# Kernel optimization log

Measured on AMD Instinct MI355X. Metric: run time of the kernel, lower is better.

## Reference

```python
import jax, jax.numpy as jnp
import numpy as np
from jax import lax

B, L, D_MODEL = 2, 1024, 2048
D_INNER, D_STATE, D_CONV, DT_RANK = 4096, 16, 4, 128
EPS = 1e-5


def setup_inputs() -> dict:
    key = jax.random.key(0)
    ks = jax.random.split(key, 10)
    sc = lambda k, shape, s=0.02: jax.random.normal(k, shape, jnp.float32) * s
    # A initialized like real Mamba: A_log = log(arange(1, d_state+1))
    A_log = jnp.log(jnp.broadcast_to(jnp.arange(1, D_STATE + 1, dtype=jnp.float32), (D_INNER, D_STATE)))
    return {
        "hidden_states": jax.random.normal(ks[0], (B, L, D_MODEL), jnp.float32),
        "residual": jax.random.normal(ks[1], (B, L, D_MODEL), jnp.float32),
        "norm_weight": jnp.ones((D_MODEL,), jnp.float32),
        "in_proj_w": sc(ks[2], (2 * D_INNER, D_MODEL)),
        "conv_w": sc(ks[3], (D_INNER, D_CONV), 0.1),
        "conv_b": jnp.zeros((D_INNER,), jnp.float32),
        "x_proj_w": sc(ks[4], (DT_RANK + 2 * D_STATE, D_INNER)),
        "dt_proj_w": sc(ks[5], (D_INNER, DT_RANK), 0.1),
        "dt_proj_b": sc(ks[6], (D_INNER,), 0.5),
        "A_log": A_log,
        "D_param": jnp.ones((D_INNER,), jnp.float32),
        "out_proj_w": sc(ks[7], (D_MODEL, D_INNER)),
    }


def _rmsnorm(x, w, eps=EPS):
    var = jnp.mean(jnp.square(x), axis=-1, keepdims=True)
    return x * lax.rsqrt(var + eps) * w


def _mamba_block(hidden_states, residual, norm_weight, in_proj_w, conv_w, conv_b,
                 x_proj_w, dt_proj_w, dt_proj_b, A_log, D_param, out_proj_w):
    # fused add + RMSNorm, residual kept in fp32 (prenorm=True)
    residual = (hidden_states + residual).astype(jnp.float32)
    hs = _rmsnorm(residual, norm_weight)

    # ---- Mamba mixer ----
    xz = jnp.einsum("bld,ed->ble", hs, in_proj_w)          # [B,L,2*d_inner]
    x, z = jnp.split(xz, 2, axis=-1)                        # each [B,L,d_inner]

    # depthwise causal conv over time
    xt = x.swapaxes(1, 2)                                   # [B,d_inner,L]
    xt = lax.conv_general_dilated(
        xt, conv_w[:, None, :], window_strides=(1,), padding=[(D_CONV - 1, 0)],
        dimension_numbers=("NCH", "OIH", "NCH"), feature_group_count=D_INNER)
    xt = xt + conv_b[:, None]
    x = jax.nn.silu(xt).swapaxes(1, 2)                      # [B,L,d_inner]

    # input-dependent dt, B, C
    x_dbl = jnp.einsum("bld,ed->ble", x, x_proj_w)          # [B,L,dt_rank+2*d_state]
    dt, Bm, Cm = jnp.split(x_dbl, [DT_RANK, DT_RANK + D_STATE], axis=-1)
    dt = jax.nn.softplus(jnp.einsum("blr,dr->bld", dt, dt_proj_w) + dt_proj_b)  # [B,L,d_inner]

    A = -jnp.exp(A_log)                                     # [d_inner,d_state]

    # selective scan: h_t = exp(dt_t*A) h_{t-1} + dt_t*B_t*x_t ; y_t = <h_t, C_t>
    def step(h, inp):
        dt_t, x_t, B_t, C_t = inp                           # [B,di],[B,di],[B,ds],[B,ds]
        dA = jnp.exp(dt_t[:, :, None] * A)                  # [B,di,ds]
        h = dA * h + (dt_t * x_t)[:, :, None] * B_t[:, None, :]
        y = jnp.einsum("bds,bs->bd", h, C_t)
        return h, y

    xs = (dt.swapaxes(0, 1), x.swapaxes(0, 1), Bm.swapaxes(0, 1), Cm.swapaxes(0, 1))
    h0 = jnp.zeros((B, D_INNER, D_STATE), jnp.float32)
    _, ys = lax.scan(step, h0, xs)                          # ys: [L,B,d_inner]
    y = ys.swapaxes(0, 1) + x * D_param                     # [B,L,d_inner]

    y = y * jax.nn.silu(z)
    out = jnp.einsum("bld,ed->ble", y, out_proj_w)          # [B,L,d_model]
    return out, residual


def reference(hidden_states, residual, norm_weight, in_proj_w, conv_w, conv_b,
              x_proj_w, dt_proj_w, dt_proj_b, A_log, D_param, out_proj_w):
    return _mamba_block(hidden_states, residual, norm_weight, in_proj_w, conv_w,
                        conv_b, x_proj_w, dt_proj_w, dt_proj_b, A_log, D_param,
                        out_proj_w)
```

## Files before the change

### kernel.cpp

```cpp
#include <hip/hip_runtime.h>
#include <hip/hip_bf16.h>
#include <math.h>

#define B_SZ    2
#define L_SZ    1024
#define DMODEL  2048
#define DINNER  4096
#define DSTATE  16
#define DCONV   4
#define DTRANK  128
#define NROWS   (B_SZ * L_SZ)
#define NCHUNK  16
#define CHUNKLEN (L_SZ / NCHUNK)

typedef __hip_bfloat16 bf16;
typedef __attribute__((ext_vector_type(8))) short  short8;
typedef __attribute__((ext_vector_type(4))) float  floatx4;

static __device__ __forceinline__ float b2f(bf16 v) { return __bfloat162float(v); }
static __device__ __forceinline__ bf16  f2b(float v) { return __float2bfloat16(v); }

static __device__ __forceinline__ void cvt8(const short8 v, float* out) {
    #pragma unroll
    for (int i = 0; i < 8; i++) {
        unsigned int u = ((unsigned int)(unsigned short)v[i]) << 16;
        out[i] = __builtin_bit_cast(float, u);
    }
}

static __device__ __forceinline__ float softplus_safe(float x) {
    return fmaxf(x, 0.f) + log1pf(__expf(-fabsf(x)));
}

static __device__ __forceinline__ void gload_lds16(const bf16* g, bf16* l) {
    __builtin_amdgcn_global_load_lds(
        (const __attribute__((address_space(1))) void*)g,
        (__attribute__((address_space(3))) void*)l,
        16, 0, 0);
}

__global__ void probe_kernel(const void* nw, int* flag) {
    if (threadIdx.x == 0 && blockIdx.x == 0) {
        const unsigned short* p = (const unsigned short*)nw;
        *flag = (p[0] == 0x3F80u) ? 0 : 1;
    }
}
__global__ void assert_fp32_kernel(const int* flag, float* out) {
    if (*flag == 0) out[blockIdx.x * 256 + threadIdx.x] = 888.0f;
}
__global__ void fill_diag_kernel(unsigned short* out, int n) {
    int i = blockIdx.x * 256 + threadIdx.x;
    if (i < n) out[i] = 0x4442;
}

__global__ __launch_bounds__(256) void cvt_w_kernel(
    const float* __restrict__ in, bf16* __restrict__ out, int n)
{
    int i = (blockIdx.x * 256 + threadIdx.x) * 4;
    if (i < n) {
        float4 v = *(const float4*)(in + i);
        out[i + 0] = f2b(v.x); out[i + 1] = f2b(v.y);
        out[i + 2] = f2b(v.z); out[i + 3] = f2b(v.w);
    }
}

__global__ __launch_bounds__(256) void addnorm_kernel(
    const float* __restrict__ h, const float* __restrict__ r,
    const float* __restrict__ w, bf16* __restrict__ hs_out)
{
    const int row = blockIdx.x;
    const int t   = threadIdx.x;
    const size_t base = (size_t)row * DMODEL;

    float vals[8];
    float ss = 0.f;
    #pragma unroll
    for (int i = 0; i < 8; i++) {
        int c = t + i * 256;
        float v = h[base + c] + r[base + c];
        vals[i] = v;
        ss += v * v;
    }
    #pragma unroll
    for (int off = 32; off > 0; off >>= 1) ss += __shfl_down(ss, off);
    __shared__ float wsum[4];
    if ((t & 63) == 0) wsum[t >> 6] = ss;
    __syncthreads();
    float tot = wsum[0] + wsum[1] + wsum[2] + wsum[3];
    float scale = rsqrtf(tot / (float)DMODEL + 1e-5f);

    #pragma unroll
    for (int i = 0; i < 8; i++) {
        int c = t + i * 256;
        hs_out[base + c] = f2b(vals[i] * scale * w[c]);
    }
}

__global__ __launch_bounds__(256) void residual_out_kernel(
    const float* __restrict__ h, const float* __restrict__ r,
    float* __restrict__ resp)
{
    int i = (blockIdx.x * 256 + threadIdx.x) * 4;
    float4 a = *(const float4*)(h + i);
    float4 b = *(const float4*)(r + i);
    float4 o = {a.x + b.x, a.y + b.y, a.z + b.z, a.w + b.w};
    *(float4*)(resp + i) = o;
}

__global__ __launch_bounds__(256) void addf_kernel(
    float* __restrict__ outp, const float* __restrict__ c1)
{
    int i = (blockIdx.x * 256 + threadIdx.x) * 4;
    float4 a = *(const float4*)(outp + i);
    float4 b = *(const float4*)(c1 + i);
    float4 o = {a.x + b.x, a.y + b.y, a.z + b.z, a.w + b.w};
    *(float4*)(outp + i) = o;
}

__global__ __launch_bounds__(512, 2) void gemm_bigtile(
    const bf16* __restrict__ A, const bf16* __restrict__ B,
    bf16* __restrict__ C, int N, int K, int lda, int ldb, int ldc)
{
    __shared__ bf16 sA[4][8192];
    __shared__ bf16 sB[4][8192];

    const int t     = threadIdx.x;
    const int lane  = t & 63;
    const int w     = t >> 6;
    const int wm    = w & 1;
    const int wn    = w >> 1;
    const int idx16 = lane & 15;
    const int quad  = lane >> 4;

    const int tilesN = N >> 8;
    const int m_blk  = (blockIdx.x / tilesN) << 8;
    const int n_blk  = (blockIdx.x % tilesN) << 8;

    const int srow  = t >> 2;
    const int sslot = t & 3;
    const int gswz  = ((sslot ^ ((srow >> 1) & 3)) << 3);
    const bf16* gA = A + (size_t)(m_blk + srow) * lda + gswz;
    const bf16* gB = B + (size_t)(n_blk + srow) * ldb + gswz;

    bf16* ldsA = &sA[0][0] + (w << 9);
    bf16* ldsB = &sB[0][0] + (w << 9);

    const int rswz = ((quad ^ ((idx16 >> 1) & 3)) << 3);
    const int aoff = ((wm << 7) + idx16) * 32 + rswz;
    const int boff = ((wn << 6) + idx16) * 32 + rswz;

#define STAGE_A(tt) do { const int _r = (tt) & 3; const size_t _k = (size_t)(tt) << 5; \
    gload_lds16(gA + _k,                      ldsA + _r * 8192); \
    gload_lds16(gA + ((size_t)lda << 7) + _k, ldsA + _r * 8192 + 4096); } while (0)
#define STAGE_B(tt) do { const int _r = (tt) & 3; const size_t _k = (size_t)(tt) << 5; \
    gload_lds16(gB + _k,                      ldsB + _r * 8192); \
    gload_lds16(gB + ((size_t)ldb << 7) + _k, ldsB + _r * 8192 + 4096); } while (0)

    floatx4 acc[8][4] = {};
    const int NT = K >> 5;

    STAGE_A(0); STAGE_B(0);
    STAGE_A(1); STAGE_B(1);
    STAGE_A(2); STAGE_B(2);
    asm volatile("s_waitcnt vmcnt(8)" ::: "memory");
    __builtin_amdgcn_s_barrier();
    __builtin_amdgcn_sched_barrier(0);

    #pragma unroll 1
    for (int tt = 0; tt < NT; ++tt) {
        const bf16* la = &sA[tt & 3][0] + aoff;
        const bf16* lb = &sB[tt & 3][0] + boff;

        short8 af[4], bfr[4];
        #pragma unroll
        for (int i = 0; i < 4; i++) af[i]  = *(const short8*)(la + i * 512);
        #pragma unroll
        for (int j = 0; j < 4; j++) bfr[j] = *(const short8*)(lb + j * 512);
        if (tt + 3 < NT) STAGE_A(tt + 3);
        asm volatile("s_waitcnt lgkmcnt(0)" ::: "memory");
        __builtin_amdgcn_sched_barrier(0);
        __builtin_amdgcn_s_setprio(1);
        #pragma unroll
        for (int i = 0; i < 4; i++)
            #pragma unroll
            for (int j = 0; j < 4; j++)
                acc[i][j] = __builtin_amdgcn_mfma_f32_16x16x32_bf16(
                    af[i], bfr[j], acc[i][j], 0, 0, 0);
        __builtin_amdgcn_s_setprio(0);

        short8 ag[4];
        #pragma unroll
        for (int i = 0; i < 4; i++) ag[i] = *(const short8*)(la + (i + 4) * 512);
        if (tt + 3 < NT) STAGE_B(tt + 3);
        asm volatile("s_waitcnt lgkmcnt(0)" ::: "memory");
        __builtin_amdgcn_sched_barrier(0);
        __builtin_amdgcn_s_setprio(1);
        #pragma unroll
        for (int i = 0; i < 4; i++)
            #pragma unroll
            for (int j = 0; j < 4; j++)
                acc[i + 4][j] = __builtin_amdgcn_mfma_f32_16x16x32_bf16(
                    ag[i], bfr[j], acc[i + 4][j], 0, 0, 0);
        __builtin_amdgcn_s_setprio(0);

        const int ahead = NT - 1 - tt;
        if (ahead >= 3)      asm volatile("s_waitcnt vmcnt(8)" ::: "memory");
        else if (ahead == 2) asm volatile("s_waitcnt vmcnt(4)" ::: "memory");
        else if (ahead == 1) asm volatile("s_waitcnt vmcnt(0)" ::: "memory");
        if (ahead > 0) {
            __builtin_amdgcn_s_barrier();
            __builtin_amdgcn_sched_barrier(0);
        }
    }
#undef STAGE_A
#undef STAGE_B

    #pragma unroll
    for (int i = 0; i < 8; i++) {
        #pragma unroll
        for (int j = 0; j < 4; j++) {
            const int r0 = m_blk + (wm << 7) + i * 16 + quad * 4;
            const int c  = n_blk + (wn << 6) + j * 16 + idx16;
            #pragma unroll
            for (int rr = 0; rr < 4; rr++)
                C[(size_t)(r0 + rr) * ldc + c] = f2b(acc[i][j][rr]);
        }
    }
}

__global__ __launch_bounds__(256) void gemm_lds_sk2(
    const bf16* __restrict__ A, const bf16* __restrict__ B,
    float* __restrict__ C0, float* __restrict__ C1)
{
    __shared__ bf16 As[128 * 32];
    __shared__ bf16 Bs[128 * 32];

    const int t    = threadIdx.x;
    const int lane = t & 63;
    const int wave = t >> 6;
    const int ks   = blockIdx.x >> 8;
    const int bid  = blockIdx.x & 255;
    const int m_blk = (bid >> 4) * 128;
    const int n_blk = (bid & 15) * 128;
    const int kbase = ks * 2048;

    const int idx16 = lane & 15;
    const int quad  = lane >> 4;
    const int wm = (wave & 1) * 64;
    const int wn = (wave >> 1) * 64;

    const int row_s = t >> 2;
    const int koff  = ((t & 3) ^ ((row_s >> 1) & 3)) * 8;
    const bf16* gA = A + (size_t)(m_blk + row_s) * 4096 + koff + kbase;
    const bf16* gB = B + (size_t)(n_blk + row_s) * 4096 + koff + kbase;
    bf16* lA = As + wave * 512;
    bf16* lB = Bs + wave * 512;

    const int rswz = (quad ^ ((idx16 >> 1) & 3)) * 8;

    floatx4 acc[4][4] = {};

    for (int k0 = 0; k0 < 2048; k0 += 32) {
        gload_lds16(gA + k0,                    lA);
        gload_lds16(gA + (size_t)64 * 4096 + k0, lA + 2048);
        gload_lds16(gB + k0,                    lB);
        gload_lds16(gB + (size_t)64 * 4096 + k0, lB + 2048);
        __syncthreads();

        short8 af[4], bfr[4];
        #pragma unroll
        for (int i = 0; i < 4; i++)
            af[i]  = *(const short8*)(As + (wm + i * 16 + idx16) * 32 + rswz);
        #pragma unroll
        for (int j = 0; j < 4; j++)
            bfr[j] = *(const short8*)(Bs + (wn + j * 16 + idx16) * 32 + rswz);
        #pragma unroll
        for (int i = 0; i < 4; i++)
            #pragma unroll
            for (int j = 0; j < 4; j++)
                acc[i][j] = __builtin_amdgcn_mfma_f32_16x16x32_bf16(
                    af[i], bfr[j], acc[i][j], 0, 0, 0);
        __syncthreads();
    }

    float* C = ks ? C1 : C0;
    #pragma unroll
    for (int i = 0; i < 4; i++) {
        #pragma unroll
        for (int j = 0; j < 4; j++) {
            const int r0 = m_blk + wm + i * 16 + quad * 4;
            const int c  = n_blk + wn + j * 16 + idx16;
            #pragma unroll
            for (int r = 0; r < 4; r++)
                C[(size_t)(r0 + r) * DMODEL + c] = acc[i][j][r];
        }
    }
}

__global__ __launch_bounds__(256) void gemm_g2_sk(
    const bf16* __restrict__ x, const bf16* __restrict__ W,
    float* __restrict__ part)
{
    const int lane = threadIdx.x & 63;
    const int gw   = blockIdx.x * 4 + (threadIdx.x >> 6);
    const int tile = gw >> 2;
    const int s    = gw & 3;
    const int wm = tile / 10;
    const int wn = tile % 10;
    const int idx16 = lane & 15, quad = lane >> 4;
    const int k0 = s * 1024;

    floatx4 acc = {};
    const bf16* Ap = x + (size_t)(wm * 16 + idx16) * DINNER + quad * 8 + k0;
    const bf16* Bp = W + (size_t)(wn * 16 + idx16) * DINNER + quad * 8 + k0;
    for (int k = 0; k < 1024; k += 32) {
        short8 af  = *(const short8*)(Ap + k);
        short8 bfr = *(const short8*)(Bp + k);
        acc = __builtin_amdgcn_mfma_f32_16x16x32_bf16(af, bfr, acc, 0, 0, 0);
    }
    #pragma unroll
    for (int r = 0; r < 4; r++)
        part[((size_t)s * NROWS + wm * 16 + quad * 4 + r) * 160 + wn * 16 + idx16]
            = acc[r];
}

__global__ __launch_bounds__(256) void g2_reduce_kernel(
    const float* __restrict__ part, bf16* __restrict__ xdbl)
{
    int i = blockIdx.x * 256 + threadIdx.x;
    float v = part[i] + part[327680 + i] + part[2 * 327680 + i]
            + part[3 * 327680 + i];
    xdbl[i] = f2b(v);
}

__global__ __launch_bounds__(256) void gemm_g3_direct(
    const bf16* __restrict__ xdbl, const bf16* __restrict__ W,
    const float* __restrict__ bias, bf16* __restrict__ dtout)
{
    const int lane = threadIdx.x & 63;
    const int gw   = blockIdx.x * 4 + (threadIdx.x >> 6);
    const int wm = gw >> 8;
    const int wn = gw & 255;
    const int idx16 = lane & 15, quad = lane >> 4;

    floatx4 acc = {};
    const bf16* Ap = xdbl + (size_t)(wm * 16 + idx16) * 160 + quad * 8;
    const bf16* Bp = W + (size_t)(wn * 16 + idx16) * DTRANK + quad * 8;
    #pragma unroll
    for (int k = 0; k < 128; k += 32) {
        short8 af  = *(const short8*)(Ap + k);
        short8 bfr = *(const short8*)(Bp + k);
        acc = __builtin_amdgcn_mfma_f32_16x16x32_bf16(af, bfr, acc, 0, 0, 0);
    }
    const int c = wn * 16 + idx16;
    const float bv = bias[c];
    #pragma unroll
    for (int r = 0; r < 4; r++)
        dtout[(size_t)(wm * 16 + quad * 4 + r) * (2 * DINNER) + c]
            = f2b(softplus_safe(acc[r] + bv));
}

__global__ __launch_bounds__(256) void conv_silu_kernel(
    const bf16* __restrict__ xz, const float* __restrict__ cw,
    const float* __restrict__ cb, bf16* __restrict__ xout)
{
    const int idx = (blockIdx.x * 256 + threadIdx.x) * 8;
    const int d0 = idx & (DINNER - 1);
    const int bl = idx >> 12;
    const int l  = bl & (L_SZ - 1);
    const int b  = bl >> 10;

    float acc[8];
    {
        float4 c0 = *(const float4*)(cb + d0);
        float4 c1 = *(const float4*)(cb + d0 + 4);
        acc[0] = c0.x; acc[1] = c0.y; acc[2] = c0.z; acc[3] = c0.w;
        acc[4] = c1.x; acc[5] = c1.y; acc[6] = c1.z; acc[7] = c1.w;
    }
    floatx4 cwv[8];
    #pragma unroll
    for (int i = 0; i < 8; i++)
        cwv[i] = *(const floatx4*)(cw + (size_t)(d0 + i) * DCONV);

    #pragma unroll
    for (int t = 0; t < DCONV; t++) {
        int ls = l - (DCONV - 1) + t;
        if (ls >= 0) {
            short8 v = *(const short8*)(xz + ((size_t)(b * L_SZ + ls)) * (2 * DINNER) + d0);
            float xf[8]; cvt8(v, xf);
            #pragma unroll
            for (int i = 0; i < 8; i++) acc[i] += cwv[i][t] * xf[i];
        }
    }
    short8 o;
    #pragma unroll
    for (int i = 0; i < 8; i++) {
        float s = acc[i] / (1.f + __expf(-acc[i]));
        o[i] = (short)__builtin_bit_cast(unsigned short, f2b(s));
    }
    *(short8*)(xout + idx) = o;
}

__global__ __launch_bounds__(256) void scan_part1(
    const bf16* __restrict__ xz, const bf16* __restrict__ x,
    const bf16* __restrict__ xdbl, const float* __restrict__ A_log,
    float* __restrict__ hpart, float* __restrict__ dtsum)
{
    __shared__ float sBC[64 * 32];
    const int tid = threadIdx.x, bid = blockIdx.x;
    const int sub = tid & 1;
    const int d   = ((bid & 31) << 7) + (tid >> 1);
    const int b   = (bid >> 5) & 1;
    const int c   = bid >> 6;
    const size_t row0 = (size_t)b * L_SZ + c * CHUNKLEN;

    {
        int r = tid >> 2, sl = tid & 3;
        short8 v = *(const short8*)(xdbl + (row0 + r) * 160 + DTRANK + sl * 8);
        float tmp[8]; cvt8(v, tmp);
        #pragma unroll
        for (int i = 0; i < 8; i++) sBC[r * 32 + sl * 8 + i] = tmp[i];
    }
    __syncthreads();

    float Aa[8];
    #pragma unroll
    for (int s = 0; s < 8; s++)
        Aa[s] = -__expf(A_log[d * DSTATE + sub * 8 + s]);

    float h[8] = {};
    float dts = 0.f;
    const floatx4* BC4 = (const floatx4*)sBC;
    const int bc0 = sub * 2;

    #pragma unroll 1
    for (int l0 = 0; l0 < CHUNKLEN; l0 += 4) {
        float dtv[4], xv[4];
        #pragma unroll
        for (int u = 0; u < 4; u++) {
            const size_t rbl = row0 + l0 + u;
            dtv[u] = b2f(xz[rbl * (2 * DINNER) + d]);
            xv[u]  = b2f(x[rbl * DINNER + d]);
        }
        #pragma unroll
        for (int u = 0; u < 4; u++) {
            const int l = l0 + u;
            floatx4 B0 = BC4[l * 8 + bc0];
            floatx4 B1 = BC4[l * 8 + bc0 + 1];
            dts += dtv[u];
            float dx = dtv[u] * xv[u];
            #pragma unroll
            for (int s = 0; s < 4; s++)
                h[s] = __expf(dtv[u] * Aa[s]) * h[s] + dx * B0[s];
            #pragma unroll
            for (int s = 0; s < 4; s++)
                h[s + 4] = __expf(dtv[u] * Aa[s + 4]) * h[s + 4] + dx * B1[s];
        }
    }
    const size_t sbase = ((size_t)((b * DINNER + d) * NCHUNK + c)) * 16 + sub * 8;
    *(floatx4*)(hpart + sbase)     = (floatx4){h[0], h[1], h[2], h[3]};
    *(floatx4*)(hpart + sbase + 4) = (floatx4){h[4], h[5], h[6], h[7]};
    if (!sub) dtsum[(b * DINNER + d) * NCHUNK + c] = dts;
}

__global__ __launch_bounds__(256) void scan_part2(
    const float* __restrict__ A_log, float* hpart,
    const float* __restrict__ dtsum)
{
    const int t = blockIdx.x * 256 + threadIdx.x;
    const int s = t & 15;
    const int d = (t >> 4) & (DINNER - 1);
    const int b = t >> 16;
    const float Aa = -__expf(A_log[d * DSTATE + s]);
    const size_t base = (size_t)(b * DINNER + d) * NCHUNK;
    float h = 0.f;
    #pragma unroll
    for (int c = 0; c < NCHUNK; c++) {
        float tmp = hpart[(base + c) * 16 + s];
        hpart[(base + c) * 16 + s] = h;
        h = __expf(Aa * dtsum[base + c]) * h + tmp;
    }
}

__global__ __launch_bounds__(256) void scan_part3(
    const bf16* __restrict__ xz, const bf16* x,
    const bf16* __restrict__ xdbl, const float* __restrict__ A_log,
    const float* __restrict__ Dp, const float* __restrict__ hpart,
    bf16* y)
{
    __shared__ float sBC[64 * 32];
    const int tid = threadIdx.x, bid = blockIdx.x;
    const int sub = tid & 1;
    const int d   = ((bid & 31) << 7) + (tid >> 1);
    const int b   = (bid >> 5) & 1;
    const int c   = bid >> 6;
    const size_t row0 = (size_t)b * L_SZ + c * CHUNKLEN;

    {
        int r = tid >> 2, sl = tid & 3;
        short8 v = *(const short8*)(xdbl + (row0 + r) * 160 + DTRANK + sl * 8);
        float tmp[8]; cvt8(v, tmp);
        #pragma unroll
        for (int i = 0; i < 8; i++) sBC[r * 32 + sl * 8 + i] = tmp[i];
    }
    __syncthreads();

    float Aa[8];
    #pragma unroll
    for (int s = 0; s < 8; s++)
        Aa[s] = -__expf(A_log[d * DSTATE + sub * 8 + s]);
    const float Dv = Dp[d];

    float h[8];
    const size_t sbase = ((size_t)((b * DINNER + d) * NCHUNK + c)) * 16 + sub * 8;
    {
        floatx4 h0 = *(const floatx4*)(hpart + sbase);
        floatx4 h1 = *(const floatx4*)(hpart + sbase + 4);
        #pragma unroll
        for (int s = 0; s < 4; s++) { h[s] = h0[s]; h[s + 4] = h1[s]; }
    }

    const floatx4* BC4 = (const floatx4*)sBC;
    const int bc0 = sub * 2;

    #pragma unroll 1
    for (int l0 = 0; l0 < CHUNKLEN; l0 += 4) {
        float dtv[4], xv[4], zv[4];
        #pragma unroll
        for (int u = 0; u < 4; u++) {
            const size_t rbl = row0 + l0 + u;
            dtv[u] = b2f(xz[rbl * (2 * DINNER) + d]);
            xv[u]  = b2f(x[rbl * DINNER + d]);
            zv[u]  = b2f(xz[rbl * (2 * DINNER) + DINNER + d]);
        }
        #pragma unroll
        for (int u = 0; u < 4; u++) {
            const int l = l0 + u;
            floatx4 B0 = BC4[l * 8 + bc0];
            floatx4 B1 = BC4[l * 8 + bc0 + 1];
            floatx4 C0 = BC4[l * 8 + 4 + bc0];
            floatx4 C1 = BC4[l * 8 + 4 + bc0 + 1];
            float dx = dtv[u] * xv[u];
            float ys = 0.f;
            #pragma unroll
            for (int s = 0; s < 4; s++) {
                h[s] = __expf(dtv[u] * Aa[s]) * h[s] + dx * B0[s];
                ys += h[s] * C0[s];
            }
            #pragma unroll
            for (int s = 0; s < 4; s++) {
                h[s + 4] = __expf(dtv[u] * Aa[s + 4]) * h[s + 4] + dx * B1[s];
                ys += h[s + 4] * C1[s];
            }
            ys += __shfl_xor(ys, 1);
            if (!sub) {
                const size_t rbl = row0 + l;
                float sig = zv[u] / (1.f + __expf(-zv[u]));
                y[rbl * DINNER + d] = f2b((ys + xv[u] * Dv) * sig);
            }
        }
    }
}

extern "C" void kernel_launch(void* const* d_in, const int* in_sizes, int n_in,
                              void* d_out, int out_size, void* d_ws, size_t ws_size,
                              hipStream_t stream)
{
    const size_t WS_NEED = 33554432ull + 16777216ull + 655360ull + 4ull;
    if (ws_size < WS_NEED) {
        fill_diag_kernel<<<(out_size + 255) / 256, 256, 0, stream>>>(
            (unsigned short*)d_out, out_size);
        return;
    }

    char* ws = (char*)d_ws;
    bf16*  xz    = (bf16*)(ws);
    float* c1    = (float*)(ws);
    bf16*  hs    = (bf16*)(ws + 33554432);
    bf16*  x     = (bf16*)(ws + 33554432);
    bf16*  y     = x;
    bf16*  xdbl  = (bf16*)(ws + 50331648);
    int*   flag  = (int*)(ws + 50987008);

    char* od = (char*)d_out;
    bf16*  w1bf  = (bf16*)od;
    bf16*  wdtbf = (bf16*)od;
    bf16*  wxbf  = (bf16*)(od + 1048576);
    float* dtsum = (float*)(od + 2359296);
    float* hpart = (float*)(od + 2883584);
    float* g2part= (float*)(od + 11272192);
    bf16*  wobf  = (bf16*)(od + 16777216);
    float* outp  = (float*)d_out;
    float* resp  = (float*)d_out + (size_t)NROWS * DMODEL;

    const float* hid = (const float*)d_in[0];
    const float* res = (const float*)d_in[1];
    const float* nw  = (const float*)d_in[2];
    const float* w1  = (const float*)d_in[3];
    const float* cw  = (const float*)d_in[4];
    const float* cb  = (const float*)d_in[5];
    const float* wx  = (const float*)d_in[6];
    const float* wdt = (const float*)d_in[7];
    const float* bdt = (const float*)d_in[8];
    const float* Al  = (const float*)d_in[9];
    const float* Dp  = (const float*)d_in[10];
    const float* wo  = (const float*)d_in[11];

    probe_kernel<<<1, 64, 0, stream>>>(d_in[2], flag);

    addnorm_kernel<<<NROWS, 256, 0, stream>>>(hid, res, nw, hs);
    cvt_w_kernel<<<(2 * DINNER * DMODEL) / 1024, 256, 0, stream>>>(
        w1, w1bf, 2 * DINNER * DMODEL);
    gemm_bigtile<<<(2048 / 256) * (8192 / 256), 512, 0, stream>>>(
        hs, w1bf, xz, 2 * DINNER, DMODEL, DMODEL, DMODEL, 2 * DINNER);

    cvt_w_kernel<<<(DINNER * DTRANK) / 1024, 256, 0, stream>>>(
        wdt, wdtbf, DINNER * DTRANK);
    cvt_w_kernel<<<(160 * DINNER) / 1024, 256, 0, stream>>>(
        wx, wxbf, 160 * DINNER);
    cvt_w_kernel<<<(DMODEL * DINNER) / 1024, 256, 0, stream>>>(
        wo, wobf, DMODEL * DINNER);

    conv_silu_kernel<<<(NROWS * DINNER) / 2048, 256, 0, stream>>>(xz, cw, cb, x);

    gemm_g2_sk<<<1280, 256, 0, stream>>>(x, wxbf, g2part);
    g2_reduce_kernel<<<(NROWS * 160) / 256, 256, 0, stream>>>(g2part, xdbl);

    gemm_g3_direct<<<8192, 256, 0, stream>>>(xdbl, wdtbf, bdt, xz);

    scan_part1<<<(NCHUNK * B_SZ * DINNER * 2) / 256, 256, 0, stream>>>(
        xz, x, xdbl, Al, hpart, dtsum);
    scan_part2<<<(B_SZ * DINNER * DSTATE) / 256, 256, 0, stream>>>(
        Al, hpart, dtsum);
    scan_part3<<<(NCHUNK * B_SZ * DINNER * 2) / 256, 256, 0, stream>>>(
        xz, x, xdbl, Al, Dp, hpart, y);

    gemm_lds_sk2<<<512, 256, 0, stream>>>(y, wobf, outp, c1);
    addf_kernel<<<(NROWS * DMODEL) / 1024, 256, 0, stream>>>(outp, c1);

    residual_out_kernel<<<(NROWS * DMODEL) / 1024, 256, 0, stream>>>(
        hid, res, resp);

    assert_fp32_kernel<<<16, 256, 0, stream>>>(flag, outp);
}
```

Before: 493.5 us.

## Software-pipeline LDS fragment loads across k-tiles with double-buffered registers

Restructures the GEMM main loop to unroll by two and prefetch the next k-tile's A/B fragments from LDS into a second register set while MFMAs on the current tile run. Global-to-LDS staging for both A and B is issued together at the start of each half-step, and the barrier moves between the two MFMA halves. The goal is to hide LDS read latency behind tensor-core work, at the cost of more VGPR pressure and an assumption that NT is even.

```diff
diff --git a/kernel.cpp b/kernel.cpp
--- a/kernel.cpp
+++ b/kernel.cpp
@@ -166,50 +166,98 @@
     __builtin_amdgcn_s_barrier();
     __builtin_amdgcn_sched_barrier(0);
 
+    short8 afX[4], bfX[4], afY[4], bfY[4], ag[4];
+    {
+        const bf16* la = &sA[0][0] + aoff;
+        const bf16* lb = &sB[0][0] + boff;
+        #pragma unroll
+        for (int i = 0; i < 4; i++) afX[i] = *(const short8*)(la + i * 512);
+        #pragma unroll
+        for (int j = 0; j < 4; j++) bfX[j] = *(const short8*)(lb + j * 512);
+    }
+
     #pragma unroll 1
-    for (int tt = 0; tt < NT; ++tt) {
-        const bf16* la = &sA[tt & 3][0] + aoff;
-        const bf16* lb = &sB[tt & 3][0] + boff;
-
-        short8 af[4], bfr[4];
-        #pragma unroll
-        for (int i = 0; i < 4; i++) af[i]  = *(const short8*)(la + i * 512);
-        #pragma unroll
-        for (int j = 0; j < 4; j++) bfr[j] = *(const short8*)(lb + j * 512);
-        if (tt + 3 < NT) STAGE_A(tt + 3);
-        asm volatile("s_waitcnt lgkmcnt(0)" ::: "memory");
-        __builtin_amdgcn_sched_barrier(0);
-        __builtin_amdgcn_s_setprio(1);
-        #pragma unroll
-        for (int i = 0; i < 4; i++)
-            #pragma unroll
-            for (int j = 0; j < 4; j++)
-                acc[i][j] = __builtin_amdgcn_mfma_f32_16x16x32_bf16(
-                    af[i], bfr[j], acc[i][j], 0, 0, 0);
-        __builtin_amdgcn_s_setprio(0);
-
-        short8 ag[4];
-        #pragma unroll
-        for (int i = 0; i < 4; i++) ag[i] = *(const short8*)(la + (i + 4) * 512);
-        if (tt + 3 < NT) STAGE_B(tt + 3);
-        asm volatile("s_waitcnt lgkmcnt(0)" ::: "memory");
-        __builtin_amdgcn_sched_barrier(0);
-        __builtin_amdgcn_s_setprio(1);
-        #pragma unroll
-        for (int i = 0; i < 4; i++)
-            #pragma unroll
-            for (int j = 0; j < 4; j++)
-                acc[i + 4][j] = __builtin_amdgcn_mfma_f32_16x16x32_bf16(
-                    ag[i], bfr[j], acc[i + 4][j], 0, 0, 0);
-        __builtin_amdgcn_s_setprio(0);
-
-        const int ahead = NT - 1 - tt;
-        if (ahead >= 3)      asm volatile("s_waitcnt vmcnt(8)" ::: "memory");
-        else if (ahead == 2) asm volatile("s_waitcnt vmcnt(4)" ::: "memory");
-        else if (ahead == 1) asm volatile("s_waitcnt vmcnt(0)" ::: "memory");
-        if (ahead > 0) {
+    for (int tt = 0; tt < NT; tt += 2) {
+        {
+            const bf16* la = &sA[tt & 3][0] + aoff;
+            if (tt + 3 < NT) { STAGE_A(tt + 3); STAGE_B(tt + 3); }
+            #pragma unroll
+            for (int i = 0; i < 4; i++) ag[i] = *(const short8*)(la + (i + 4) * 512);
+
+            __builtin_amdgcn_s_setprio(1);
+            #pragma unroll
+            for (int i = 0; i < 4; i++)
+                #pragma unroll
+                for (int j = 0; j < 4; j++)
+                    acc[i][j] = __builtin_amdgcn_mfma_f32_16x16x32_bf16(
+                        afX[i], bfX[j], acc[i][j], 0, 0, 0);
+            __builtin_amdgcn_s_setprio(0);
+
+            asm volatile("s_waitcnt lgkmcnt(0)" ::: "memory");
+            __builtin_amdgcn_sched_barrier(0);
+            const int ahead = NT - 1 - tt;
+            if (ahead >= 3)      asm volatile("s_waitcnt vmcnt(8)" ::: "memory");
+            else if (ahead == 2) asm volatile("s_waitcnt vmcnt(4)" ::: "memory");
+            else                 asm volatile("s_waitcnt vmcnt(0)" ::: "memory");
             __builtin_amdgcn_s_barrier();
             __builtin_amdgcn_sched_barrier(0);
+
+            const bf16* la2 = &sA[(tt + 1) & 3][0] + aoff;
+            const bf16* lb2 = &sB[(tt + 1) & 3][0] + boff;
+            #pragma unroll
+            for (int i = 0; i < 4; i++) afY[i] = *(const short8*)(la2 + i * 512);
+            #pragma unroll
+            for (int j = 0; j < 4; j++) bfY[j] = *(const short8*)(lb2 + j * 512);
+
+            __builtin_amdgcn_s_setprio(1);
+            #pragma unroll
+            for (int i = 0; i < 4; i++)
+                #pragma unroll
+                for (int j = 0; j < 4; j++)
+                    acc[i + 4][j] = __builtin_amdgcn_mfma_f32_16x16x32_bf16(
+                        ag[i], bfX[j], acc[i + 4][j], 0, 0, 0);
+            __builtin_amdgcn_s_setprio(0);
+        }
+        {
+            const bf16* la = &sA[(tt + 1) & 3][0] + aoff;
+            if (tt + 4 < NT) { STAGE_A(tt + 4); STAGE_B(tt + 4); }
+            #pragma unroll
+            for (int i = 0; i < 4; i++) ag[i] = *(const short8*)(la + (i + 4) * 512);
+
+            __builtin_amdgcn_s_setprio(1);
+            #pragma unroll
+            for (int i = 0; i < 4; i++)
+                #pragma unroll
+                for (int j = 0; j < 4; j++)
+                    acc[i][j] = __builtin_amdgcn_mfma_f32_16x16x32_bf16(
+                        afY[i], bfY[j], acc[i][j], 0, 0, 0);
+            __builtin_amdgcn_s_setprio(0);
+
+            asm volatile("s_waitcnt lgkmcnt(0)" ::: "memory");
+            __builtin_amdgcn_sched_barrier(0);
+            const int ahead2 = NT - 2 - tt;
+            if (ahead2 >= 3)      asm volatile("s_waitcnt vmcnt(8)" ::: "memory");
+            else if (ahead2 == 2) asm volatile("s_waitcnt vmcnt(4)" ::: "memory");
+            else if (ahead2 == 1) asm volatile("s_waitcnt vmcnt(0)" ::: "memory");
+            if (ahead2 > 0) {
+                __builtin_amdgcn_s_barrier();
+                __builtin_amdgcn_sched_barrier(0);
+                const bf16* la2 = &sA[(tt + 2) & 3][0] + aoff;
+                const bf16* lb2 = &sB[(tt + 2) & 3][0] + boff;
+                #pragma unroll
+                for (int i = 0; i < 4; i++) afX[i] = *(const short8*)(la2 + i * 512);
+                #pragma unroll
+                for (int j = 0; j < 4; j++) bfX[j] = *(const short8*)(lb2 + j * 512);
+            }
+
+            __builtin_amdgcn_s_setprio(1);
+            #pragma unroll
+            for (int i = 0; i < 4; i++)
+                #pragma unroll
+                for (int j = 0; j < 4; j++)
+                    acc[i + 4][j] = __builtin_amdgcn_mfma_f32_16x16x32_bf16(
+                        ag[i], bfY[j], acc[i + 4][j], 0, 0, 0);
+            __builtin_amdgcn_s_setprio(0);
         }
     }
 #undef STAGE_A
```

New measurement: 488.2 us. About the same (-1.1%).
